# Kernel optimization log

Hardware: AMD Instinct MI355X
Metric: run time of the kernel (lower is better)

## Reference

```python
import jax, jax.numpy as jnp
import numpy as np

TEMP = 0.1
EPS = 0.5
N, D, P = 8192, 128, 1


def setup_inputs() -> dict:
    key = jax.random.key(0)
    k1, k2 = jax.random.split(key)
    return {
        "embeddings": jax.random.normal(k1, (N, D), dtype=jnp.float32),
        "properties": jax.random.uniform(k2, (N, P), dtype=jnp.float32),
    }


def reference(embeddings, properties):
    n = embeddings.shape[0]
    # L2-normalize rows, cosine similarity scaled by temperature
    e = embeddings / jnp.linalg.norm(embeddings, axis=1, keepdims=True)
    sim = (e @ e.T) / TEMP  # [N, N]

    # mask from property distances; comparison is non-differentiable in torch,
    # so stop_gradient keeps the jax graph identical (and avoids sqrt(0) nans)
    props = jax.lax.stop_gradient(properties)
    pd2 = jnp.sum((props[:, None, :] - props[None, :, :]) ** 2, axis=-1)  # [N, N]
    # torch.cdist(p=2) gives sqrt(pd2); code then takes .sqrt() again -> pd2**0.25
    prop_dists = jnp.sqrt(jnp.sqrt(pd2)) + 1e-8
    mask = (prop_dists < EPS).astype(sim.dtype)

    eye = jnp.eye(n, dtype=bool)
    mask = jnp.where(eye, 0.0, mask)          # fill_diagonal_(0)
    logits = jnp.where(eye, -1e9, sim)        # fill_diagonal_(-1e9)
    log_probs = jax.nn.log_softmax(logits, axis=1)

    # fused masked per-row mean of -log_probs over positives, then mean over
    # rows that have at least one positive (replaces the python loop)
    counts = mask.sum(axis=1)                      # [N]
    valid = counts > 0
    per_row = -(mask * log_probs).sum(axis=1) / jnp.maximum(counts, 1.0)
    n_valid = valid.sum()
    loss = jnp.where(
        n_valid > 0,
        jnp.sum(jnp.where(valid, per_row, 0.0)) / jnp.maximum(n_valid, 1).astype(per_row.dtype),
        jnp.asarray(0.0, dtype=per_row.dtype),
    )
    return loss
```

## Files before the change

kernel.cpp:

```cpp
#include <hip/hip_runtime.h>
#include <hip/hip_bf16.h>

#define N_ROWS 8192
#define DIM 128

typedef short v8s __attribute__((ext_vector_type(8)));
typedef float v4f __attribute__((ext_vector_type(4)));
typedef unsigned int u32;

constexpr int NS = 16;
constexpr int CW = N_ROWS / NS;
constexpr int NSLOT = NS;
constexpr int TILE_J = 64;
constexpr int NTILE = CW / TILE_J;
constexpr int TILE_BYTES = TILE_J * DIM * 2;
constexpr float THRESH = 0.25f;
constexpr float C1 = 14.426950408889634f;

#define GLDS(gptr, lptr, sz)                                                   \
  __builtin_amdgcn_global_load_lds(                                            \
      (const __attribute__((address_space(1))) u32*)(gptr),                    \
      (__attribute__((address_space(3))) u32*)(lptr), sz, 0, 0)

__device__ __forceinline__ unsigned short f2bf(float f) {
  __hip_bfloat16 h = __float2bfloat16(f);
  return __builtin_bit_cast(unsigned short, h);
}

__global__ __launch_bounds__(256) void knorm(const float* __restrict__ emb,
                                             unsigned short* __restrict__ ebf) {
  const int row  = blockIdx.x * 4 + (threadIdx.x >> 6);
  const int lane = threadIdx.x & 63;
  const float2 v = *reinterpret_cast<const float2*>(emb + (size_t)row * DIM + lane * 2);
  float ss = fmaf(v.x, v.x, v.y * v.y);
#pragma unroll
  for (int off = 32; off > 0; off >>= 1) ss += __shfl_xor(ss, off);
  const float rn = 1.0f / sqrtf(ss);
  const unsigned int packed =
      (unsigned int)f2bf(v.x * rn) | ((unsigned int)f2bf(v.y * rn) << 16);
  *reinterpret_cast<unsigned int*>(ebf + (size_t)row * DIM + lane * 2) = packed;
}

__global__ __launch_bounds__(256) void kmain(const unsigned short* __restrict__ ebf,
                                             const float* __restrict__ props,
                                             float* __restrict__ part) {
  const int lane = threadIdx.x & 63;
  const int w    = threadIdx.x >> 6;
  const int l15  = lane & 15;
  const int g    = lane >> 4;
  const int i0   = blockIdx.x * 128;
  const int iw0  = i0 + w * 32;
  const int jbase = blockIdx.y * CW;
  const int kb   = g * 8;

  __shared__ __align__(1024) char sA[2 * TILE_BYTES + CW * 4];
  char* sprops = sA + 2 * TILE_BYTES;

  const int icol0 = iw0 + l15;
  const int icol1 = iw0 + 16 + l15;

  v8s bfr0[4], bfr1[4];
#pragma unroll
  for (int k = 0; k < 4; ++k) {
    bfr0[k] = *reinterpret_cast<const v8s*>(ebf + (size_t)icol0 * DIM + k * 32 + kb);
    bfr1[k] = *reinterpret_cast<const v8s*>(ebf + (size_t)icol1 * DIM + k * 32 + kb);
  }
  const float pc0 = props[icol0];
  const float pc1 = props[icol1];

#pragma unroll
  for (int r = 0; r < 2; ++r)
    GLDS(props + jbase + r * 256 + w * 64 + lane, sprops + r * 1024 + w * 256, 4);

  auto stageA = [&](int buf, int tile) {
    const int jrow0 = jbase + tile * TILE_J;
    char* base = sA + buf * TILE_BYTES;
#pragma unroll
    for (int q = 0; q < 4; ++q) {
      const int row  = q * 16 + w * 4 + g;
      const int colb = (l15 << 4) ^ ((row & 7) << 4);
      GLDS(ebf + (size_t)(jrow0 + row) * DIM + (colb >> 1),
           base + q * 4096 + w * 1024, 16);
    }
  };

  float es0 = 0.f, es1 = 0.f, ms0 = 0.f, ms1 = 0.f, ct0 = 0.f, ct1 = 0.f;

  stageA(0, 0);
  __syncthreads();

  int cur = 0;
  for (int t = 0; t < NTILE; ++t) {
    if (t + 1 < NTILE) stageA(cur ^ 1, t + 1);

    char* base = sA + cur * TILE_BYTES;
    const int swz = (l15 & 7) << 4;
#pragma unroll
    for (int s = 0; s < 4; ++s) {
      const int jrow0 = jbase + t * TILE_J + s * 16;
      const int row   = s * 16 + l15;
      v8s af[4];
#pragma unroll
      for (int k = 0; k < 4; ++k)
        af[k] = *reinterpret_cast<const v8s*>(base + row * 256 + ((k * 64 + g * 16) ^ swz));
      const float4 pj = *reinterpret_cast<const float4*>(sprops + t * 256 + s * 64 + g * 16);

      v4f acc0 = {0.f, 0.f, 0.f, 0.f}, acc1 = {0.f, 0.f, 0.f, 0.f};
#pragma unroll
      for (int k = 0; k < 4; ++k) {
        acc0 = __builtin_amdgcn_mfma_f32_16x16x32_bf16(af[k], bfr0[k], acc0, 0, 0, 0);
        acc1 = __builtin_amdgcn_mfma_f32_16x16x32_bf16(af[k], bfr1[k], acc1, 0, 0, 0);
      }

      const float pjv[4] = {pj.x, pj.y, pj.z, pj.w};
      if ((unsigned)(jrow0 - i0) < 128u) {
#pragma unroll
        for (int r = 0; r < 4; ++r) {
          const int jr = jrow0 + g * 4 + r;
          {
            const float dot = acc0[r];
            const bool  neq = (jr != icol0);
            const float ex  = __builtin_amdgcn_exp2f(fmaf(dot, C1, -C1));
            es0 += neq ? ex : 0.f;
            const float mskf = (neq && (fabsf(pc0 - pjv[r]) < THRESH)) ? 1.f : 0.f;
            ct0 += mskf;
            ms0 = fmaf(mskf, dot, ms0);
          }
          {
            const float dot = acc1[r];
            const bool  neq = (jr != icol1);
            const float ex  = __builtin_amdgcn_exp2f(fmaf(dot, C1, -C1));
            es1 += neq ? ex : 0.f;
            const float mskf = (neq && (fabsf(pc1 - pjv[r]) < THRESH)) ? 1.f : 0.f;
            ct1 += mskf;
            ms1 = fmaf(mskf, dot, ms1);
          }
        }
      } else {
#pragma unroll
        for (int r = 0; r < 4; ++r) {
          {
            const float dot = acc0[r];
            es0 += __builtin_amdgcn_exp2f(fmaf(dot, C1, -C1));
            const float mskf = (fabsf(pc0 - pjv[r]) < THRESH) ? 1.f : 0.f;
            ct0 += mskf;
            ms0 = fmaf(mskf, dot, ms0);
          }
          {
            const float dot = acc1[r];
            es1 += __builtin_amdgcn_exp2f(fmaf(dot, C1, -C1));
            const float mskf = (fabsf(pc1 - pjv[r]) < THRESH) ? 1.f : 0.f;
            ct1 += mskf;
            ms1 = fmaf(mskf, dot, ms1);
          }
        }
      }
    }
    __syncthreads();
    cur ^= 1;
  }

#pragma unroll
  for (int off = 16; off <= 32; off <<= 1) {
    es0 += __shfl_xor(es0, off);  es1 += __shfl_xor(es1, off);
    ms0 += __shfl_xor(ms0, off);  ms1 += __shfl_xor(ms1, off);
    ct0 += __shfl_xor(ct0, off);  ct1 += __shfl_xor(ct1, off);
  }

  if (g == 0) {
    float* p0 = part + (size_t)blockIdx.y * 3 * N_ROWS;
    p0[icol0]              = es0;
    p0[N_ROWS + icol0]     = ms0;
    p0[2 * N_ROWS + icol0] = ct0;
    p0[icol1]              = es1;
    p0[N_ROWS + icol1]     = ms1;
    p0[2 * N_ROWS + icol1] = ct1;
  }
}

__global__ __launch_bounds__(256) void kreduce(const float* __restrict__ part,
                                               float* __restrict__ bs,
                                               float* __restrict__ bc) {
  const int row = blockIdx.x * 256 + threadIdx.x;
  float es = 0.f, ms = 0.f, ct = 0.f;
#pragma unroll
  for (int sp = 0; sp < NSLOT; ++sp) {
    const float* p0 = part + (size_t)sp * 3 * N_ROWS;
    es += p0[row];
    ms += p0[N_ROWS + row];
    ct += p0[2 * N_ROWS + row];
  }
  const float lse = 10.0f + logf(es);
  const float per = (ct * lse - 10.0f * ms) / fmaxf(ct, 1.0f);
  float val = (ct > 0.f) ? per : 0.f;
  float vld = (ct > 0.f) ? 1.f : 0.f;
#pragma unroll
  for (int off = 32; off > 0; off >>= 1) {
    val += __shfl_xor(val, off);
    vld += __shfl_xor(vld, off);
  }
  __shared__ float sv[4], sc[4];
  const int wid = threadIdx.x >> 6;
  if ((threadIdx.x & 63) == 0) { sv[wid] = val; sc[wid] = vld; }
  __syncthreads();
  if (threadIdx.x == 0) {
    bs[blockIdx.x] = sv[0] + sv[1] + sv[2] + sv[3];
    bc[blockIdx.x] = sc[0] + sc[1] + sc[2] + sc[3];
  }
}

__global__ __launch_bounds__(64) void kfin(const float* __restrict__ bs,
                                           const float* __restrict__ bc,
                                           float* __restrict__ out) {
  const int l = threadIdx.x;
  float s = (l < 32) ? bs[l] : 0.f;
  float c = (l < 32) ? bc[l] : 0.f;
#pragma unroll
  for (int off = 32; off > 0; off >>= 1) {
    s += __shfl_xor(s, off);
    c += __shfl_xor(c, off);
  }
  if (l == 0) out[0] = (c > 0.f) ? (s / c) : 0.f;
}

extern "C" void kernel_launch(void* const* d_in, const int* in_sizes, int n_in,
                              void* d_out, int out_size, void* d_ws, size_t ws_size,
                              hipStream_t stream) {
  const float* emb   = (const float*)d_in[0];
  const float* props = (const float*)d_in[1];
  float* out = (float*)d_out;

  unsigned short* ebf = (unsigned short*)d_ws;
  const size_t EBF_BYTES  = (size_t)N_ROWS * DIM * 2;
  const size_t PART_BYTES = (size_t)NSLOT * 3 * N_ROWS * 4;
  float* part = (float*)((char*)d_ws + EBF_BYTES);
  float* bs   = (float*)((char*)d_ws + EBF_BYTES + PART_BYTES);
  float* bc   = bs + 32;

  knorm<<<N_ROWS / 4, 256, 0, stream>>>(emb, ebf);
  kmain<<<dim3(N_ROWS / 128, NS), 256, 0, stream>>>(ebf, props, part);
  kreduce<<<N_ROWS / 256, 256, 0, stream>>>(part, bs, bc);
  kfin<<<1, 64, 0, stream>>>(bs, bc, out);
}
```

Measured before the change: 46.90 us.

## Triple-buffer smaller LDS tiles with vmcnt waits and split accumulators

Halves the staged tile to 32 rows and uses a three-slot LDS ring, prefetching two tiles ahead. The full __syncthreads is replaced by explicit s_waitcnt vmcnt plus a bare s_barrier, which waits only for older direct-to-LDS loads. Per-row accumulators are split into two partial chains to shorten dependency chains. The risk is more barriers per tile and reliance on the exact vmcnt count being correct for the prop loads and tile loads.

```diff
diff --git a/kernel.cpp b/kernel.cpp
--- a/kernel.cpp
+++ b/kernel.cpp
@@ -11,9 +11,9 @@
 constexpr int NS = 16;
 constexpr int CW = N_ROWS / NS;
 constexpr int NSLOT = NS;
-constexpr int TILE_J = 64;
-constexpr int NTILE = CW / TILE_J;
-constexpr int TILE_BYTES = TILE_J * DIM * 2;
+constexpr int TILE_J = 32;
+constexpr int NT = CW / TILE_J;
+constexpr int TB = TILE_J * DIM * 2;
 constexpr float THRESH = 0.25f;
 constexpr float C1 = 14.426950408889634f;
 
@@ -53,8 +53,8 @@
   const int jbase = blockIdx.y * CW;
   const int kb   = g * 8;
 
-  __shared__ __align__(1024) char sA[2 * TILE_BYTES + CW * 4];
-  char* sprops = sA + 2 * TILE_BYTES;
+  __shared__ __align__(1024) char sA[3 * TB + CW * 4];
+  char* sprops = sA + 3 * TB;
 
   const int icol0 = iw0 + l15;
   const int icol1 = iw0 + 16 + l15;
@@ -68,15 +68,10 @@
   const float pc0 = props[icol0];
   const float pc1 = props[icol1];
 
-#pragma unroll
-  for (int r = 0; r < 2; ++r)
-    GLDS(props + jbase + r * 256 + w * 64 + lane, sprops + r * 1024 + w * 256, 4);
-
-  auto stageA = [&](int buf, int tile) {
+  auto stageA = [&](char* base, int tile) {
     const int jrow0 = jbase + tile * TILE_J;
-    char* base = sA + buf * TILE_BYTES;
-#pragma unroll
-    for (int q = 0; q < 4; ++q) {
+#pragma unroll
+    for (int q = 0; q < 2; ++q) {
       const int row  = q * 16 + w * 4 + g;
       const int colb = (l15 << 4) ^ ((row & 7) << 4);
       GLDS(ebf + (size_t)(jrow0 + row) * DIM + (colb >> 1),
@@ -84,26 +79,38 @@
     }
   };
 
-  float es0 = 0.f, es1 = 0.f, ms0 = 0.f, ms1 = 0.f, ct0 = 0.f, ct1 = 0.f;
-
-  stageA(0, 0);
-  __syncthreads();
-
-  int cur = 0;
-  for (int t = 0; t < NTILE; ++t) {
-    if (t + 1 < NTILE) stageA(cur ^ 1, t + 1);
-
-    char* base = sA + cur * TILE_BYTES;
-    const int swz = (l15 & 7) << 4;
-#pragma unroll
-    for (int s = 0; s < 4; ++s) {
+#pragma unroll
+  for (int r = 0; r < 2; ++r)
+    GLDS(props + jbase + r * 256 + w * 64 + lane, sprops + r * 1024 + w * 256, 4);
+  stageA(sA + 0 * TB, 0);
+  stageA(sA + 1 * TB, 1);
+
+  float es0a = 0.f, es0b = 0.f, es1a = 0.f, es1b = 0.f;
+  float ms0a = 0.f, ms0b = 0.f, ms1a = 0.f, ms1b = 0.f;
+  float ct0a = 0.f, ct0b = 0.f, ct1a = 0.f, ct1b = 0.f;
+
+  const int swz = (l15 & 7) << 4;
+
+  for (int t = 0; t < NT; ++t) {
+    if (t < NT - 1) {
+      asm volatile("s_waitcnt vmcnt(2)" ::: "memory");
+    } else {
+      asm volatile("s_waitcnt vmcnt(0)" ::: "memory");
+    }
+    __builtin_amdgcn_s_barrier();
+
+    if (t + 2 < NT) stageA(sA + ((t + 2) % 3) * TB, t + 2);
+
+    char* base = sA + (t % 3) * TB;
+#pragma unroll
+    for (int s = 0; s < 2; ++s) {
       const int jrow0 = jbase + t * TILE_J + s * 16;
       const int row   = s * 16 + l15;
       v8s af[4];
 #pragma unroll
       for (int k = 0; k < 4; ++k)
         af[k] = *reinterpret_cast<const v8s*>(base + row * 256 + ((k * 64 + g * 16) ^ swz));
-      const float4 pj = *reinterpret_cast<const float4*>(sprops + t * 256 + s * 64 + g * 16);
+      const float4 pj = *reinterpret_cast<const float4*>(sprops + (t * 128 + s * 64 + g * 16));
 
       v4f acc0 = {0.f, 0.f, 0.f, 0.f}, acc1 = {0.f, 0.f, 0.f, 0.f};
 #pragma unroll
@@ -117,6 +124,9 @@
 #pragma unroll
         for (int r = 0; r < 4; ++r) {
           const int jr = jrow0 + g * 4 + r;
+          float& es0 = (r & 2) ? es0b : es0a;  float& es1 = (r & 2) ? es1b : es1a;
+          float& ms0 = (r & 2) ? ms0b : ms0a;  float& ms1 = (r & 2) ? ms1b : ms1a;
+          float& ct0 = (r & 2) ? ct0b : ct0a;  float& ct1 = (r & 2) ? ct1b : ct1a;
           {
             const float dot = acc0[r];
             const bool  neq = (jr != icol0);
@@ -139,6 +149,9 @@
       } else {
 #pragma unroll
         for (int r = 0; r < 4; ++r) {
+          float& es0 = (r & 2) ? es0b : es0a;  float& es1 = (r & 2) ? es1b : es1a;
+          float& ms0 = (r & 2) ? ms0b : ms0a;  float& ms1 = (r & 2) ? ms1b : ms1a;
+          float& ct0 = (r & 2) ? ct0b : ct0a;  float& ct1 = (r & 2) ? ct1b : ct1a;
           {
             const float dot = acc0[r];
             es0 += __builtin_amdgcn_exp2f(fmaf(dot, C1, -C1));
@@ -156,9 +169,11 @@
         }
       }
     }
-    __syncthreads();
-    cur ^= 1;
-  }
+  }
+
+  float es0 = es0a + es0b, es1 = es1a + es1b;
+  float ms0 = ms0a + ms0b, ms1 = ms1a + ms1b;
+  float ct0 = ct0a + ct0b, ct1 = ct1a + ct1b;
 
 #pragma unroll
   for (int off = 16; off <= 32; off <<= 1) {
```

Result: slower. 48.57 us (+3.6%).

## Switch main similarity kernel to 32x32x16 bf16 MFMA with 32-row tiles

Applied to the files above, without the earlier changes.

Replaces the pair of 16x16x32 MFMA accumulators per wave with a single 32x32x16 bf16 MFMA accumulator covering 32 i-rows by 32 j-rows. The j tile shrinks from 64 to 32 rows, so the LDS fragment loads, property reads and the epilogue index mapping are reworked for the 32x32 output layout. Each wave now holds one i-column per lane pair, with split accumulators to shorten dependency chains. This aims to cut MFMA issue count and LDS fragment reads per FLOP, but adds twice as many loop iterations and barriers per j-range.

```diff
diff --git a/kernel.cpp b/kernel.cpp
--- a/kernel.cpp
+++ b/kernel.cpp
@@ -4,16 +4,16 @@
 #define N_ROWS 8192
 #define DIM 128
 
-typedef short v8s __attribute__((ext_vector_type(8)));
-typedef float v4f __attribute__((ext_vector_type(4)));
+typedef short v8s  __attribute__((ext_vector_type(8)));
+typedef float v16f __attribute__((ext_vector_type(16)));
 typedef unsigned int u32;
 
 constexpr int NS = 16;
 constexpr int CW = N_ROWS / NS;
 constexpr int NSLOT = NS;
-constexpr int TILE_J = 64;
-constexpr int NTILE = CW / TILE_J;
-constexpr int TILE_BYTES = TILE_J * DIM * 2;
+constexpr int TILE_J = 32;
+constexpr int NT = CW / TILE_J;
+constexpr int TB = TILE_J * DIM * 2;
 constexpr float THRESH = 0.25f;
 constexpr float C1 = 14.426950408889634f;
 
@@ -47,134 +47,109 @@
   const int lane = threadIdx.x & 63;
   const int w    = threadIdx.x >> 6;
   const int l15  = lane & 15;
-  const int g    = lane >> 4;
+  const int g4   = lane >> 4;
+  const int r31  = lane & 31;
+  const int hi   = lane >> 5;
   const int i0   = blockIdx.x * 128;
   const int iw0  = i0 + w * 32;
   const int jbase = blockIdx.y * CW;
-  const int kb   = g * 8;
-
-  __shared__ __align__(1024) char sA[2 * TILE_BYTES + CW * 4];
-  char* sprops = sA + 2 * TILE_BYTES;
-
-  const int icol0 = iw0 + l15;
-  const int icol1 = iw0 + 16 + l15;
-
-  v8s bfr0[4], bfr1[4];
-#pragma unroll
-  for (int k = 0; k < 4; ++k) {
-    bfr0[k] = *reinterpret_cast<const v8s*>(ebf + (size_t)icol0 * DIM + k * 32 + kb);
-    bfr1[k] = *reinterpret_cast<const v8s*>(ebf + (size_t)icol1 * DIM + k * 32 + kb);
-  }
-  const float pc0 = props[icol0];
-  const float pc1 = props[icol1];
+
+  __shared__ __align__(1024) char sA[2 * TB + CW * 4];
+  char* sprops = sA + 2 * TB;
+
+  const int icol = iw0 + r31;
+
+  v8s bfr[8];
+#pragma unroll
+  for (int kk = 0; kk < 8; ++kk)
+    bfr[kk] = *reinterpret_cast<const v8s*>(ebf + (size_t)icol * DIM + kk * 16 + hi * 8);
+  const float pc = props[icol];
 
 #pragma unroll
   for (int r = 0; r < 2; ++r)
     GLDS(props + jbase + r * 256 + w * 64 + lane, sprops + r * 1024 + w * 256, 4);
 
-  auto stageA = [&](int buf, int tile) {
+  auto stageA = [&](char* base, int tile) {
     const int jrow0 = jbase + tile * TILE_J;
-    char* base = sA + buf * TILE_BYTES;
-#pragma unroll
-    for (int q = 0; q < 4; ++q) {
-      const int row  = q * 16 + w * 4 + g;
+#pragma unroll
+    for (int q = 0; q < 2; ++q) {
+      const int row  = q * 16 + w * 4 + g4;
       const int colb = (l15 << 4) ^ ((row & 7) << 4);
       GLDS(ebf + (size_t)(jrow0 + row) * DIM + (colb >> 1),
            base + q * 4096 + w * 1024, 16);
     }
   };
 
-  float es0 = 0.f, es1 = 0.f, ms0 = 0.f, ms1 = 0.f, ct0 = 0.f, ct1 = 0.f;
-
-  stageA(0, 0);
+  stageA(sA, 0);
   __syncthreads();
 
-  int cur = 0;
-  for (int t = 0; t < NTILE; ++t) {
-    if (t + 1 < NTILE) stageA(cur ^ 1, t + 1);
-
-    char* base = sA + cur * TILE_BYTES;
-    const int swz = (l15 & 7) << 4;
-#pragma unroll
-    for (int s = 0; s < 4; ++s) {
-      const int jrow0 = jbase + t * TILE_J + s * 16;
-      const int row   = s * 16 + l15;
-      v8s af[4];
-#pragma unroll
-      for (int k = 0; k < 4; ++k)
-        af[k] = *reinterpret_cast<const v8s*>(base + row * 256 + ((k * 64 + g * 16) ^ swz));
-      const float4 pj = *reinterpret_cast<const float4*>(sprops + t * 256 + s * 64 + g * 16);
-
-      v4f acc0 = {0.f, 0.f, 0.f, 0.f}, acc1 = {0.f, 0.f, 0.f, 0.f};
-#pragma unroll
-      for (int k = 0; k < 4; ++k) {
-        acc0 = __builtin_amdgcn_mfma_f32_16x16x32_bf16(af[k], bfr0[k], acc0, 0, 0, 0);
-        acc1 = __builtin_amdgcn_mfma_f32_16x16x32_bf16(af[k], bfr1[k], acc1, 0, 0, 0);
+  float es2[2] = {0.f, 0.f}, ms2[2] = {0.f, 0.f}, ct2[2] = {0.f, 0.f};
+  const int rswz = (r31 & 7) << 4;
+
+  for (int t = 0; t < NT; ++t) {
+    if (t + 1 < NT) stageA(sA + ((t + 1) & 1) * TB, t + 1);
+
+    char* base = sA + (t & 1) * TB;
+    const int jrow0 = jbase + t * TILE_J;
+
+    v8s af[8];
+#pragma unroll
+    for (int kk = 0; kk < 8; ++kk)
+      af[kk] = *reinterpret_cast<const v8s*>(
+          base + r31 * 256 + ((kk * 32 + hi * 16) ^ rswz));
+
+    float pjf[16];
+#pragma unroll
+    for (int q = 0; q < 4; ++q) {
+      const float4 v = *reinterpret_cast<const float4*>(
+          sprops + t * 128 + hi * 16 + q * 32);
+      pjf[q * 4 + 0] = v.x; pjf[q * 4 + 1] = v.y;
+      pjf[q * 4 + 2] = v.z; pjf[q * 4 + 3] = v.w;
+    }
+
+    v16f acc = {0.f, 0.f, 0.f, 0.f, 0.f, 0.f, 0.f, 0.f,
+                0.f, 0.f, 0.f, 0.f, 0.f, 0.f, 0.f, 0.f};
+#pragma unroll
+    for (int kk = 0; kk < 8; ++kk)
+      acc = __builtin_amdgcn_mfma_f32_32x32x16_bf16(af[kk], bfr[kk], acc, 0, 0, 0);
+
+    if ((unsigned)(jrow0 - i0) < 128u) {
+#pragma unroll
+      for (int reg = 0; reg < 16; ++reg) {
+        const int jr = jrow0 + (reg & 3) + 8 * (reg >> 2) + 4 * hi;
+        const float dot = acc[reg];
+        const bool  neq = (jr != icol);
+        const float ex  = __builtin_amdgcn_exp2f(fmaf(dot, C1, -C1));
+        es2[reg & 1] += neq ? ex : 0.f;
+        const float mskf = (neq && (fabsf(pc - pjf[reg]) < THRESH)) ? 1.f : 0.f;
+        ct2[reg & 1] += mskf;
+        ms2[reg & 1] = fmaf(mskf, dot, ms2[reg & 1]);
       }
-
-      const float pjv[4] = {pj.x, pj.y, pj.z, pj.w};
-      if ((unsigned)(jrow0 - i0) < 128u) {
-#pragma unroll
-        for (int r = 0; r < 4; ++r) {
-          const int jr = jrow0 + g * 4 + r;
-          {
-            const float dot = acc0[r];
-            const bool  neq = (jr != icol0);
-            const float ex  = __builtin_amdgcn_exp2f(fmaf(dot, C1, -C1));
-            es0 += neq ? ex : 0.f;
-            const float mskf = (neq && (fabsf(pc0 - pjv[r]) < THRESH)) ? 1.f : 0.f;
-            ct0 += mskf;
-            ms0 = fmaf(mskf, dot, ms0);
-          }
-          {
-            const float dot = acc1[r];
-            const bool  neq = (jr != icol1);
-            const float ex  = __builtin_amdgcn_exp2f(fmaf(dot, C1, -C1));
-            es1 += neq ? ex : 0.f;
-            const float mskf = (neq && (fabsf(pc1 - pjv[r]) < THRESH)) ? 1.f : 0.f;
-            ct1 += mskf;
-            ms1 = fmaf(mskf, dot, ms1);
-          }
-        }
-      } else {
-#pragma unroll
-        for (int r = 0; r < 4; ++r) {
-          {
-            const float dot = acc0[r];
-            es0 += __builtin_amdgcn_exp2f(fmaf(dot, C1, -C1));
-            const float mskf = (fabsf(pc0 - pjv[r]) < THRESH) ? 1.f : 0.f;
-            ct0 += mskf;
-            ms0 = fmaf(mskf, dot, ms0);
-          }
-          {
-            const float dot = acc1[r];
-            es1 += __builtin_amdgcn_exp2f(fmaf(dot, C1, -C1));
-            const float mskf = (fabsf(pc1 - pjv[r]) < THRESH) ? 1.f : 0.f;
-            ct1 += mskf;
-            ms1 = fmaf(mskf, dot, ms1);
-          }
-        }
+    } else {
+#pragma unroll
+      for (int reg = 0; reg < 16; ++reg) {
+        const float dot = acc[reg];
+        es2[reg & 1] += __builtin_amdgcn_exp2f(fmaf(dot, C1, -C1));
+        const float mskf = (fabsf(pc - pjf[reg]) < THRESH) ? 1.f : 0.f;
+        ct2[reg & 1] += mskf;
+        ms2[reg & 1] = fmaf(mskf, dot, ms2[reg & 1]);
       }
     }
     __syncthreads();
-    cur ^= 1;
-  }
-
-#pragma unroll
-  for (int off = 16; off <= 32; off <<= 1) {
-    es0 += __shfl_xor(es0, off);  es1 += __shfl_xor(es1, off);
-    ms0 += __shfl_xor(ms0, off);  ms1 += __shfl_xor(ms1, off);
-    ct0 += __shfl_xor(ct0, off);  ct1 += __shfl_xor(ct1, off);
-  }
-
-  if (g == 0) {
+  }
+
+  float es = es2[0] + es2[1];
+  float ms = ms2[0] + ms2[1];
+  float ct = ct2[0] + ct2[1];
+  es += __shfl_xor(es, 32);
+  ms += __shfl_xor(ms, 32);
+  ct += __shfl_xor(ct, 32);
+
+  if (hi == 0) {
     float* p0 = part + (size_t)blockIdx.y * 3 * N_ROWS;
-    p0[icol0]              = es0;
-    p0[N_ROWS + icol0]     = ms0;
-    p0[2 * N_ROWS + icol0] = ct0;
-    p0[icol1]              = es1;
-    p0[N_ROWS + icol1]     = ms1;
-    p0[2 * N_ROWS + icol1] = ct1;
+    p0[icol]              = es;
+    p0[N_ROWS + icol]     = ms;
+    p0[2 * N_ROWS + icol] = ct;
   }
 }
 
```

Result: no change. 46.47 us (-0.9%).
